# Optimization experiments

Hardware: AMD Instinct MI355X
Metric: run time of the kernel (lower is better)

Reference implementation:

```python
import jax, jax.numpy as jnp
import numpy as np

B, N, D, H, COND = 1, 1024, 1024, 16, 128
S = 2 * N          # noisy tokens + clean x0 tokens
BS = 16            # diffusion block size
HD = D // H        # head dim = 64


def _ln(x, w):
    # LayerNorm module: F.layer_norm in fp32, then scale by weight (no bias)
    x = x.astype(jnp.float32)
    mu = jnp.mean(x, axis=-1, keepdims=True)
    var = jnp.var(x, axis=-1, keepdims=True)
    return (x - mu) / jnp.sqrt(var + 1e-5) * w


def _rotate_half(x):
    x1, x2 = jnp.split(x, 2, axis=-1)
    return jnp.concatenate([-x2, x1], axis=-1)


def _block_diff_mask(s, n, bs):
    q = jnp.arange(s)[:, None]
    k = jnp.arange(s)[None, :]
    fq = q >= n
    fk = k >= n
    bq = jnp.where(fq, (q - n) // bs, q // bs)
    bk = jnp.where(fk, (k - n) // bs, k // bs)
    diag = (bq == bk) & (fq == fk)
    off = (bq > bk) & fk & (~fq)
    caus = (bq >= bk) & fk & fq
    return diag | off | caus


def setup_inputs() -> dict:
    key = jax.random.key(0)
    ks = jax.random.split(key, 8)
    inv = 1.0 / (10000.0 ** (jnp.arange(0, HD, 2, dtype=jnp.float32) / HD))  # [32]
    t = jnp.arange(N, dtype=jnp.float32)[:, None] * inv[None, :]
    return {
        "x": jax.random.normal(ks[0], (B, S, D), jnp.float32),
        "c": jax.random.normal(ks[1], (B, COND), jnp.float32),
        "cos": jnp.cos(t),
        "sin": jnp.sin(t),
        "norm1_w": jnp.ones((D,), jnp.float32),
        "qkv_w": jax.random.normal(ks[2], (3 * D, D), jnp.float32) * (D ** -0.5),
        "attn_out_w": jax.random.normal(ks[3], (D, D), jnp.float32) * (D ** -0.5),
        "norm2_w": jnp.ones((D,), jnp.float32),
        "mlp_w1": jax.random.normal(ks[4], (4 * D, D), jnp.float32) * (D ** -0.5),
        "mlp_b1": jnp.zeros((4 * D,), jnp.float32),
        "mlp_w2": jax.random.normal(ks[5], (D, 4 * D), jnp.float32) * ((4 * D) ** -0.5),
        "mlp_b2": jnp.zeros((D,), jnp.float32),
        "adaLN_w": jax.random.normal(ks[6], (6 * D, COND), jnp.float32) * 0.02,
        "adaLN_b": jax.random.normal(ks[7], (6 * D,), jnp.float32) * 0.02,
    }


def reference(x, c, cos, sin, norm1_w, qkv_w, attn_out_w, norm2_w,
              mlp_w1, mlp_b1, mlp_w2, mlp_b2, adaLN_w, adaLN_b):
    # adaLN modulation: [B, 6D] -> six [B, 1, D] tensors
    mods = (c @ adaLN_w.T + adaLN_b)[:, None, :]
    sh_msa, sc_msa, g_msa, sh_mlp, sc_mlp, g_mlp = jnp.split(mods, 6, axis=-1)

    x_skip = x
    h = _ln(x, norm1_w) * (1 + sc_msa) + sh_msa  # modulate_fused

    # rotary tables broadcast to qkv rank 5 (torchscript path: applied to q, k AND v)
    cs = jnp.concatenate([cos, cos], axis=-1)[None, :, None, None, :]  # [1,N,1,1,HD]
    sn = jnp.concatenate([sin, sin], axis=-1)[None, :, None, None, :]

    def qkv_of(xh):  # xh: [B, N, D]
        qkv = (xh @ qkv_w.T).reshape(B, N, 3, H, HD)
        return qkv * cs + _rotate_half(qkv) * sn

    # halves processed separately (both use positions 0..N-1), then concatenated
    qkv = jnp.concatenate([qkv_of(h[:, :N]), qkv_of(h[:, N:])], axis=1)  # [B,S,3,H,HD]

    q = jnp.transpose(qkv[:, :, 0], (0, 2, 1, 3))  # [B,H,S,HD]
    k = jnp.transpose(qkv[:, :, 1], (0, 2, 1, 3))
    v = jnp.transpose(qkv[:, :, 2], (0, 2, 1, 3))

    scores = jnp.einsum('bhqd,bhkd->bhqk', q, k) / np.sqrt(HD).astype(np.float32)
    mask = _block_diff_mask(S, N, BS)  # [S,S] bool, block-diag | offset-causal | block-causal
    scores = jnp.where(mask[None, None], scores, -jnp.inf)
    attn = jax.nn.softmax(scores, axis=-1)
    o = jnp.einsum('bhqk,bhkd->bhqd', attn, v)
    o = jnp.transpose(o, (0, 2, 1, 3)).reshape(B, S, D)

    # inference bias_dropout_add_scale: gate * out + residual (dropout is identity)
    x2 = g_msa * (o @ attn_out_w.T) + x_skip
    h2 = _ln(x2, norm2_w) * (1 + sc_mlp) + sh_mlp
    m = jax.nn.gelu(h2 @ mlp_w1.T + mlp_b1, approximate=True) @ mlp_w2.T + mlp_b2
    return g_mlp * m + x2
```

## Files before the change

### kernel.cpp

```cpp
#include <hip/hip_runtime.h>
#include <math.h>

#define SS 2048
#define NN 1024
#define DD 1024
#define HH 16
#define CONDD 128

typedef unsigned short ushort;
typedef unsigned int uint;
typedef __bf16 bf16x8 __attribute__((ext_vector_type(8)));
typedef float f32x4 __attribute__((ext_vector_type(4)));
typedef short s16x4 __attribute__((ext_vector_type(4)));
typedef ushort u16x8 __attribute__((ext_vector_type(8)));

__device__ __forceinline__ float gelu_fast(float x) {
    float t = x + 0.044715f * x * x * x;
    float e = __builtin_exp2f(-2.3022081446f * t);
    return x * __builtin_amdgcn_rcpf(1.0f + e);
}

__device__ __forceinline__ ushort f2bf(float x) {
    uint u = __float_as_uint(x);
    u += 0x7fff + ((u >> 16) & 1);
    return (ushort)(u >> 16);
}

__device__ __forceinline__ float bf2f(ushort u) {
    return __uint_as_float(((uint)u) << 16);
}

__device__ __forceinline__ void gload16(const ushort* g, ushort* l) {
    __builtin_amdgcn_global_load_lds(
        (const __attribute__((address_space(1))) void*)g,
        (__attribute__((address_space(3))) void*)l, 16, 0, 0);
}

template <int N>
__device__ __forceinline__ void wait_vm() {
    if constexpr (N == 0)      asm volatile("s_waitcnt vmcnt(0)" ::: "memory");
    else if constexpr (N == 4) asm volatile("s_waitcnt vmcnt(4)" ::: "memory");
    else if constexpr (N == 6) asm volatile("s_waitcnt vmcnt(6)" ::: "memory");
    else if constexpr (N == 8) asm volatile("s_waitcnt vmcnt(8)" ::: "memory");
}

__device__ __forceinline__ f32x4 mfma16(s16x4 a, s16x4 b, f32x4 c) {
#if __has_builtin(__builtin_amdgcn_mfma_f32_16x16x16bf16_1k)
    return __builtin_amdgcn_mfma_f32_16x16x16bf16_1k(a, b, c, 0, 0, 0);
#else
    asm("v_mfma_f32_16x16x16_bf16 %0, %1, %2, %0" : "+v"(c) : "v"(a), "v"(b));
    return c;
#endif
}

__global__ void k_cast4(const float* __restrict__ s0, const float* __restrict__ s1,
                        const float* __restrict__ s2, const float* __restrict__ s3,
                        ushort* __restrict__ dst) {
    size_t gid = ((size_t)blockIdx.x * 256 + threadIdx.x) * 4;
    const float* src;
    size_t off;
    if (gid < (3ull << 20))      { src = s0; off = 0; }
    else if (gid < (4ull << 20)) { src = s1; off = 3ull << 20; }
    else if (gid < (8ull << 20)) { src = s2; off = 4ull << 20; }
    else                         { src = s3; off = 8ull << 20; }
    float4 v = *(const float4*)(src + (gid - off));
    ushort4 o = {f2bf(v.x), f2bf(v.y), f2bf(v.z), f2bf(v.w)};
    *(ushort4*)(dst + gid) = o;
}

__global__ void k_adaln(const float* __restrict__ c, const float* __restrict__ w,
                        const float* __restrict__ b, float* __restrict__ mods) {
    int o = blockIdx.x * 256 + threadIdx.x;
    float s = b[o];
    const float* wr = w + (size_t)o * CONDD;
    for (int k = 0; k < CONDD; ++k) s += c[k] * wr[k];
    mods[o] = s;
}

__global__ void k_ln_mod(const float* __restrict__ x, const float* __restrict__ w,
                         const float* __restrict__ mods, int sh_idx, int sc_idx,
                         ushort* __restrict__ out) {
    int row = blockIdx.x;
    int tid = threadIdx.x;
    const float* xr = x + (size_t)row * DD;
    float lx[4];
    float s = 0.f, s2 = 0.f;
    for (int i = 0; i < 4; ++i) {
        float v = xr[tid + i * 256];
        lx[i] = v; s += v; s2 += v * v;
    }
    __shared__ float rs[256], rs2[256];
    rs[tid] = s; rs2[tid] = s2; __syncthreads();
    for (int off = 128; off > 0; off >>= 1) {
        if (tid < off) { rs[tid] += rs[tid + off]; rs2[tid] += rs2[tid + off]; }
        __syncthreads();
    }
    float mu = rs[0] * (1.0f / DD);
    float var = rs2[0] * (1.0f / DD) - mu * mu;
    float rstd = rsqrtf(var + 1e-5f);
    const float* sh = mods + sh_idx * DD;
    const float* sc = mods + sc_idx * DD;
    ushort* orow = out + (size_t)row * DD;
    for (int i = 0; i < 4; ++i) {
        int d = tid + i * 256;
        orow[d] = f2bf((lx[i] - mu) * rstd * w[d] * (1.0f + sc[d]) + sh[d]);
    }
}

template <int TM, int TN, int MODE, typename OT>
__global__ void k_gemm_mfma(const ushort* __restrict__ A, const ushort* __restrict__ W,
                            const float* __restrict__ bias, const float* __restrict__ gate,
                            const float* __restrict__ resid, OT* __restrict__ C,
                            int M, int Nout, int K) {
    constexpr int WRows = (TN == 64) ? 2 : ((TM == 128) ? 2 : 1);
    constexpr int WCols = 4 / WRows;
    constexpr int WTM = TM / WRows, WTN = TN / WCols;
    constexpr int FM = WTM / 16, FN = WTN / 16;
    constexpr int BUFE = (TM + TN) * 64;
    constexpr int LPW = TM / 32 + TN / 32;
    __shared__ ushort lds[3 * BUFE];

    int tid = threadIdx.x;
    int lane = tid & 63, wave = tid >> 6;
    int wr = wave / WCols, wc = wave % WCols;
    int l15 = lane & 15, l4 = lane >> 4;

    int nwg = gridDim.x * gridDim.y;
    int orig = blockIdx.y * gridDim.x + blockIdx.x;
    int q = nwg >> 3, r = nwg & 7;
    int xcd = orig & 7, off = orig >> 3;
    int wgid = (xcd < r ? xcd * (q + 1) : r * (q + 1) + (xcd - r) * q) + off;
    int n0 = (wgid % gridDim.x) * TN;
    int m0 = (wgid / gridDim.x) * TM;

    f32x4 acc[FM][FN] = {};

    auto stage = [&](int buf, int k0) {
        ushort* base = lds + buf * BUFE;
#pragma unroll
        for (int i = 0; i < TM / 32; ++i) {
            int cb = (wave * (TM / 32) + i) * 64;
            int ch = cb + lane;
            int row = ch >> 3;
            int kc = (ch & 7) ^ (row & 7);
            gload16(A + (size_t)(m0 + row) * K + k0 + kc * 8, base + cb * 8);
        }
#pragma unroll
        for (int i = 0; i < TN / 32; ++i) {
            int cb = (wave * (TN / 32) + i) * 64;
            int ch = cb + lane;
            int row = ch >> 3;
            int kc = (ch & 7) ^ (row & 7);
            gload16(W + (size_t)(n0 + row) * K + k0 + kc * 8, base + TM * 64 + cb * 8);
        }
    };

    auto compute = [&](int buf) {
        const ushort* lA = lds + buf * BUFE;
        const ushort* lB = lA + TM * 64;
#pragma unroll
        for (int sub = 0; sub < 2; ++sub) {
            bf16x8 af[FM], bw[FN];
#pragma unroll
            for (int mi = 0; mi < FM; ++mi) {
                int row = wr * WTM + mi * 16 + l15;
                int pos = ((sub << 2) | l4) ^ (row & 7);
                af[mi] = *(const bf16x8*)&lA[row * 64 + pos * 8];
            }
#pragma unroll
            for (int ni = 0; ni < FN; ++ni) {
                int row = wc * WTN + ni * 16 + l15;
                int pos = ((sub << 2) | l4) ^ (row & 7);
                bw[ni] = *(const bf16x8*)&lB[row * 64 + pos * 8];
            }
#pragma unroll
            for (int mi = 0; mi < FM; ++mi)
#pragma unroll
                for (int ni = 0; ni < FN; ++ni)
                    acc[mi][ni] = __builtin_amdgcn_mfma_f32_16x16x32_bf16(
                        af[mi], bw[ni], acc[mi][ni], 0, 0, 0);
        }
    };

    int nk = K >> 6;
    stage(0, 0);
    stage(1, 64);
    for (int t = 0; t < nk; ++t) {
        if (t + 1 < nk) wait_vm<LPW>(); else wait_vm<0>();
        __builtin_amdgcn_s_barrier();
        __builtin_amdgcn_sched_barrier(0);
        if (t + 2 < nk) stage((t + 2) % 3, (t + 2) << 6);
        compute(t % 3);
    }

#pragma unroll
    for (int mi = 0; mi < FM; ++mi) {
#pragma unroll
        for (int r2 = 0; r2 < 4; ++r2) {
            int m = m0 + wr * WTM + mi * 16 + l4 * 4 + r2;
#pragma unroll
            for (int ni = 0; ni < FN; ++ni) {
                int n = n0 + wc * WTN + ni * 16 + l15;
                float v = acc[mi][ni][r2];
                if (MODE == 1) v = gate[n] * v + resid[(size_t)m * Nout + n];
                if (MODE == 2) v = gelu_fast(v + bias[n]);
                if (MODE == 3) v = gate[n] * (v + bias[n]) + resid[(size_t)m * Nout + n];
                if (sizeof(OT) == 2) C[(size_t)m * Nout + n] = (OT)f2bf(v);
                else                 C[(size_t)m * Nout + n] = (OT)v;
            }
        }
    }
}

__global__ void k_rope2(const ushort* __restrict__ qkvb, const float* __restrict__ cosT,
                        const float* __restrict__ sinT, ushort* __restrict__ qb,
                        ushort* __restrict__ kb, ushort* __restrict__ vT) {
    __shared__ ushort vt[64][65];
    int h = blockIdx.x & 15;
    int st = blockIdx.x >> 4;
    int s0 = st * 64;
    int tid = threadIdx.x;
#pragma unroll
    for (int i = 0; i < 8; ++i) {
        int idx = tid + i * 256;
        int sl = idx >> 5, j = idx & 31;
        int s = s0 + sl;
        int pos = s & (NN - 1);
        float cv = cosT[pos * 32 + j], sv = sinT[pos * 32 + j];
        const ushort* row = qkvb + (size_t)s * 3072 + h * 64;
        float x1 = bf2f(row[j]), x2 = bf2f(row[j + 32]);
        qb[(size_t)s * DD + h * 64 + j]      = f2bf((x1 * cv - x2 * sv) * 0.18033688011f);
        qb[(size_t)s * DD + h * 64 + j + 32] = f2bf((x2 * cv + x1 * sv) * 0.18033688011f);
        x1 = bf2f(row[1024 + j]); x2 = bf2f(row[1024 + j + 32]);
        kb[(size_t)s * DD + h * 64 + j]      = f2bf(x1 * cv - x2 * sv);
        kb[(size_t)s * DD + h * 64 + j + 32] = f2bf(x2 * cv + x1 * sv);
        x1 = bf2f(row[2048 + j]); x2 = bf2f(row[2048 + j + 32]);
        vt[sl][j]      = f2bf(x1 * cv - x2 * sv);
        vt[sl][j + 32] = f2bf(x2 * cv + x1 * sv);
    }
    __syncthreads();
    int drow = tid >> 2, sc = (tid & 3) * 16;
    u16x8 a, b;
#pragma unroll
    for (int i = 0; i < 8; ++i) { a[i] = vt[sc + i][drow]; b[i] = vt[sc + 8 + i][drow]; }
    size_t base = (size_t)(h * 64 + drow) * SS + s0 + sc;
    *(u16x8*)&vT[base] = a;
    *(u16x8*)&vT[base + 8] = b;
}

struct KVTile { bf16x8 k0, k1; s16x4 v0, v1, v2, v3; };

__global__ __launch_bounds__(256) void k_attn4(
        const ushort* __restrict__ qb, const ushort* __restrict__ kb,
        const ushort* __restrict__ vT, ushort* __restrict__ o) {
    __shared__ float Ml[2][4][16], Ll[2][4][16];
    __shared__ float Ob[2][4][16][68];

    int id = blockIdx.x;
    int h = id & 15;
    int bq = 63 - (id >> 4);
    int tid = threadIdx.x;
    int wave = tid >> 6;
    int lane = tid & 63;
    int l15 = lane & 15, l4 = lane >> 4;
    int hb = h * 64;

    const int q0A = bq * 16, q0B = NN + bq * 16;
    bf16x8 qA0 = *(const bf16x8*)&qb[(size_t)(q0A + l15) * DD + hb + l4 * 8];
    bf16x8 qA1 = *(const bf16x8*)&qb[(size_t)(q0A + l15) * DD + hb + 32 + l4 * 8];
    bf16x8 qB0 = *(const bf16x8*)&qb[(size_t)(q0B + l15) * DD + hb + l4 * 8];
    bf16x8 qB1 = *(const bf16x8*)&qb[(size_t)(q0B + l15) * DD + hb + 32 + l4 * 8];

    float mA = -1e30f, lA = 0.f, mB = -1e30f, lB = 0.f;
    f32x4 oA0 = {}, oA1 = {}, oA2 = {}, oA3 = {};
    f32x4 oB0 = {}, oB1 = {}, oB2 = {}, oB3 = {};

    auto loadT = [&](int kbase) {
        KVTile t;
        const ushort* kr = kb + (size_t)(kbase + l15) * DD + hb + l4 * 8;
        t.k0 = *(const bf16x8*)kr;
        t.k1 = *(const bf16x8*)(kr + 32);
        const ushort* vr = vT + (size_t)(hb + l15) * SS + kbase + l4 * 4;
        t.v0 = *(const s16x4*)vr;
        t.v1 = *(const s16x4*)(vr + 16 * SS);
        t.v2 = *(const s16x4*)(vr + 32 * SS);
        t.v3 = *(const s16x4*)(vr + 48 * SS);
        return t;
    };

    auto step = [&](const KVTile& t, bf16x8 Q0, bf16x8 Q1, float& m, float& l,
                    f32x4& O0, f32x4& O1, f32x4& O2, f32x4& O3) {
        f32x4 s = {};
        s = __builtin_amdgcn_mfma_f32_16x16x32_bf16(t.k0, Q0, s, 0, 0, 0);
        s = __builtin_amdgcn_mfma_f32_16x16x32_bf16(t.k1, Q1, s, 0, 0, 0);
        float tm = fmaxf(fmaxf(s[0], s[1]), fmaxf(s[2], s[3]));
        tm = fmaxf(tm, __shfl_xor(tm, 16));
        tm = fmaxf(tm, __shfl_xor(tm, 32));
        if (!__all(tm <= m + 8.0f)) {
            float mn = fmaxf(m, tm);
            float alpha = exp2f(m - mn);
            l *= alpha;
            O0 *= alpha; O1 *= alpha; O2 *= alpha; O3 *= alpha;
            m = mn;
        }
        float p0 = exp2f(s[0] - m), p1 = exp2f(s[1] - m);
        float p2 = exp2f(s[2] - m), p3 = exp2f(s[3] - m);
        float rsum = (p0 + p1) + (p2 + p3);
        rsum += __shfl_xor(rsum, 16);
        rsum += __shfl_xor(rsum, 32);
        l += rsum;
        s16x4 pf;
        pf[0] = (short)f2bf(p0); pf[1] = (short)f2bf(p1);
        pf[2] = (short)f2bf(p2); pf[3] = (short)f2bf(p3);
        O0 = mfma16(t.v0, pf, O0);
        O1 = mfma16(t.v1, pf, O1);
        O2 = mfma16(t.v2, pf, O2);
        O3 = mfma16(t.v3, pf, O3);
    };

    if (wave == 0) {
        KVTile td = loadT(q0A);
        step(td, qA0, qA1, mA, lA, oA0, oA1, oA2, oA3);
    }
    KVTile cur, nxt;
    if (wave <= bq) cur = loadT(NN + wave * 16);
    for (int t = wave; t <= bq; t += 4) {
        int tn = t + 4;
        if (tn <= bq) nxt = loadT(NN + tn * 16);
        if (t < bq) step(cur, qA0, qA1, mA, lA, oA0, oA1, oA2, oA3);
        step(cur, qB0, qB1, mB, lB, oB0, oB1, oB2, oB3);
        cur = nxt;
    }

    if (l4 == 0) {
        Ml[0][wave][l15] = mA; Ll[0][wave][l15] = lA;
        Ml[1][wave][l15] = mB; Ll[1][wave][l15] = lB;
    }
    *(f32x4*)&Ob[0][wave][l15][l4 * 4]      = oA0;
    *(f32x4*)&Ob[0][wave][l15][l4 * 4 + 16] = oA1;
    *(f32x4*)&Ob[0][wave][l15][l4 * 4 + 32] = oA2;
    *(f32x4*)&Ob[0][wave][l15][l4 * 4 + 48] = oA3;
    *(f32x4*)&Ob[1][wave][l15][l4 * 4]      = oB0;
    *(f32x4*)&Ob[1][wave][l15][l4 * 4 + 16] = oB1;
    *(f32x4*)&Ob[1][wave][l15][l4 * 4 + 32] = oB2;
    *(f32x4*)&Ob[1][wave][l15][l4 * 4 + 48] = oB3;
    __syncthreads();

    int s = tid >> 7;
    int qr = (tid >> 3) & 15;
    int db = (tid & 7) * 8;
    float m0 = Ml[s][0][qr], m1 = Ml[s][1][qr], m2 = Ml[s][2][qr], m3 = Ml[s][3][qr];
    float ms = fmaxf(fmaxf(m0, m1), fmaxf(m2, m3));
    float a0 = exp2f(m0 - ms), a1 = exp2f(m1 - ms);
    float a2 = exp2f(m2 - ms), a3 = exp2f(m3 - ms);
    float lt = a0 * Ll[s][0][qr] + a1 * Ll[s][1][qr] + a2 * Ll[s][2][qr] + a3 * Ll[s][3][qr];
    float inv = 1.0f / lt;
    int q0s = (s == 0) ? q0A : q0B;
    u16x8 outv;
#pragma unroll
    for (int j = 0; j < 8; ++j) {
        float v = a0 * Ob[s][0][qr][db + j] + a1 * Ob[s][1][qr][db + j] +
                  a2 * Ob[s][2][qr][db + j] + a3 * Ob[s][3][qr][db + j];
        outv[j] = f2bf(v * inv);
    }
    *(u16x8*)&o[(size_t)(q0s + qr) * DD + hb + db] = outv;
}

extern "C" void kernel_launch(void* const* d_in, const int* in_sizes, int n_in,
                              void* d_out, int out_size, void* d_ws, size_t ws_size,
                              hipStream_t stream) {
    const float* x          = (const float*)d_in[0];
    const float* c          = (const float*)d_in[1];
    const float* cosT       = (const float*)d_in[2];
    const float* sinT       = (const float*)d_in[3];
    const float* norm1_w    = (const float*)d_in[4];
    const float* qkv_w      = (const float*)d_in[5];
    const float* attn_out_w = (const float*)d_in[6];
    const float* norm2_w    = (const float*)d_in[7];
    const float* mlp_w1     = (const float*)d_in[8];
    const float* mlp_b1     = (const float*)d_in[9];
    const float* mlp_w2     = (const float*)d_in[10];
    const float* mlp_b2     = (const float*)d_in[11];
    const float* adaLN_w    = (const float*)d_in[12];
    const float* adaLN_b    = (const float*)d_in[13];
    float* out = (float*)d_out;

    char* p = (char*)d_ws;
    float*  mods = (float*)p;   p += 6 * DD * 4;
    ushort* qkvb = (ushort*)p;  p += (size_t)SS * 3 * DD * 2;
    ushort* qb   = (ushort*)p;  p += (size_t)SS * DD * 2;
    ushort* kb   = (ushort*)p;  p += (size_t)SS * DD * 2;
    ushort* vT   = (ushort*)p;  p += (size_t)SS * DD * 2;
    float*  x2   = (float*)p;   p += (size_t)SS * DD * 4;
    ushort* hbuf = (ushort*)p;  p += (size_t)SS * DD * 2;
    ushort* obuf = (ushort*)p;  p += (size_t)SS * DD * 2;
    ushort* wq   = (ushort*)p;  p += (size_t)3 * DD * DD * 2;
    ushort* wo   = (ushort*)p;  p += (size_t)DD * DD * 2;
    ushort* w1   = (ushort*)p;  p += (size_t)4 * DD * DD * 2;
    ushort* w2   = (ushort*)p;  p += (size_t)4 * DD * DD * 2;
    ushort* m1   = qkvb;

    k_cast4<<<(12 << 20) / 1024, 256, 0, stream>>>(qkv_w, attn_out_w, mlp_w1, mlp_w2, wq);

    k_adaln<<<6 * DD / 256, 256, 0, stream>>>(c, adaLN_w, adaLN_b, mods);
    k_ln_mod<<<SS, 256, 0, stream>>>(x, norm1_w, mods, 0, 1, hbuf);

    dim3 g1(3 * DD / 128, SS / 64);
    k_gemm_mfma<64, 128, 0, ushort><<<g1, 256, 0, stream>>>(
        hbuf, wq, nullptr, nullptr, nullptr, qkvb, SS, 3 * DD, DD);
    k_rope2<<<512, 256, 0, stream>>>(qkvb, cosT, sinT, qb, kb, vT);
    k_attn4<<<HH * 64, 256, 0, stream>>>(qb, kb, vT, obuf);

    dim3 g2(DD / 64, SS / 64);
    k_gemm_mfma<64, 64, 1, float><<<g2, 256, 0, stream>>>(
        obuf, wo, nullptr, mods + 2 * DD, x, x2, SS, DD, DD);
    k_ln_mod<<<SS, 256, 0, stream>>>(x2, norm2_w, mods, 3, 4, hbuf);

    dim3 g3(4 * DD / 128, SS / 64);
    k_gemm_mfma<64, 128, 2, ushort><<<g3, 256, 0, stream>>>(
        hbuf, w1, mlp_b1, nullptr, nullptr, m1, SS, 4 * DD, DD);
    dim3 g4(DD / 64, SS / 64);
    k_gemm_mfma<64, 64, 3, float><<<g4, 256, 0, stream>>>(
        m1, w2, mlp_b2, mods + 5 * DD, x2, out, SS, DD, 4 * DD);
}
```

Measured before the change: 162.2 us.

## Use 8-wave GEMM workgroups and store attention residual as bf16

The GEMM kernel now runs 512 threads (2x4 waves) per workgroup, so each wave owns a smaller output sub-tile and issues fewer staging loads per K-step. The wait counts are adjusted to match. The intermediate residual x2 is written as bf16 instead of fp32, which halves its write traffic and the reads by the second LayerNorm and the final GEMM. In exchange the residual stream loses precision, and smaller per-wave tiles reduce MFMA reuse per LDS fragment load.

```diff
diff --git a/kernel.cpp b/kernel.cpp
--- a/kernel.cpp
+++ b/kernel.cpp
@@ -30,6 +30,9 @@
     return __uint_as_float(((uint)u) << 16);
 }
 
+__device__ __forceinline__ float ldf(const float* p) { return *p; }
+__device__ __forceinline__ float ldf(const ushort* p) { return bf2f(*p); }
+
 __device__ __forceinline__ void gload16(const ushort* g, ushort* l) {
     __builtin_amdgcn_global_load_lds(
         (const __attribute__((address_space(1))) void*)g,
@@ -39,9 +42,8 @@
 template <int N>
 __device__ __forceinline__ void wait_vm() {
     if constexpr (N == 0)      asm volatile("s_waitcnt vmcnt(0)" ::: "memory");
-    else if constexpr (N == 4) asm volatile("s_waitcnt vmcnt(4)" ::: "memory");
-    else if constexpr (N == 6) asm volatile("s_waitcnt vmcnt(6)" ::: "memory");
-    else if constexpr (N == 8) asm volatile("s_waitcnt vmcnt(8)" ::: "memory");
+    else if constexpr (N == 2) asm volatile("s_waitcnt vmcnt(2)" ::: "memory");
+    else if constexpr (N == 3) asm volatile("s_waitcnt vmcnt(3)" ::: "memory");
 }
 
 __device__ __forceinline__ f32x4 mfma16(s16x4 a, s16x4 b, f32x4 c) {
@@ -77,16 +79,17 @@
     mods[o] = s;
 }
 
-__global__ void k_ln_mod(const float* __restrict__ x, const float* __restrict__ w,
+template <typename IT>
+__global__ void k_ln_mod(const IT* __restrict__ x, const float* __restrict__ w,
                          const float* __restrict__ mods, int sh_idx, int sc_idx,
                          ushort* __restrict__ out) {
     int row = blockIdx.x;
     int tid = threadIdx.x;
-    const float* xr = x + (size_t)row * DD;
+    const IT* xr = x + (size_t)row * DD;
     float lx[4];
     float s = 0.f, s2 = 0.f;
     for (int i = 0; i < 4; ++i) {
-        float v = xr[tid + i * 256];
+        float v = ldf(&xr[tid + i * 256]);
         lx[i] = v; s += v; s2 += v * v;
     }
     __shared__ float rs[256], rs2[256];
@@ -108,21 +111,20 @@
 }
 
 template <int TM, int TN, int MODE, typename OT>
-__global__ void k_gemm_mfma(const ushort* __restrict__ A, const ushort* __restrict__ W,
-                            const float* __restrict__ bias, const float* __restrict__ gate,
-                            const float* __restrict__ resid, OT* __restrict__ C,
-                            int M, int Nout, int K) {
-    constexpr int WRows = (TN == 64) ? 2 : ((TM == 128) ? 2 : 1);
-    constexpr int WCols = 4 / WRows;
-    constexpr int WTM = TM / WRows, WTN = TN / WCols;
+__global__ __launch_bounds__(512) void k_gemm_mfma(
+        const ushort* __restrict__ A, const ushort* __restrict__ W,
+        const float* __restrict__ bias, const float* __restrict__ gate,
+        const void* __restrict__ resid, OT* __restrict__ C,
+        int M, int Nout, int K) {
+    constexpr int WTM = TM / 2, WTN = TN / 4;
     constexpr int FM = WTM / 16, FN = WTN / 16;
     constexpr int BUFE = (TM + TN) * 64;
-    constexpr int LPW = TM / 32 + TN / 32;
+    constexpr int LPW = TM / 64 + TN / 64;
     __shared__ ushort lds[3 * BUFE];
 
     int tid = threadIdx.x;
     int lane = tid & 63, wave = tid >> 6;
-    int wr = wave / WCols, wc = wave % WCols;
+    int wr = wave >> 2, wc = wave & 3;
     int l15 = lane & 15, l4 = lane >> 4;
 
     int nwg = gridDim.x * gridDim.y;
@@ -138,16 +140,16 @@
     auto stage = [&](int buf, int k0) {
         ushort* base = lds + buf * BUFE;
 #pragma unroll
-        for (int i = 0; i < TM / 32; ++i) {
-            int cb = (wave * (TM / 32) + i) * 64;
+        for (int i = 0; i < TM / 64; ++i) {
+            int cb = (wave * (TM / 64) + i) * 64;
             int ch = cb + lane;
             int row = ch >> 3;
             int kc = (ch & 7) ^ (row & 7);
             gload16(A + (size_t)(m0 + row) * K + k0 + kc * 8, base + cb * 8);
         }
 #pragma unroll
-        for (int i = 0; i < TN / 32; ++i) {
-            int cb = (wave * (TN / 32) + i) * 64;
+        for (int i = 0; i < TN / 64; ++i) {
+            int cb = (wave * (TN / 64) + i) * 64;
             int ch = cb + lane;
             int row = ch >> 3;
             int kc = (ch & 7) ^ (row & 7);
@@ -193,6 +195,8 @@
         compute(t % 3);
     }
 
+    const float*  rf = (const float*)resid;
+    const ushort* rb = (const ushort*)resid;
 #pragma unroll
     for (int mi = 0; mi < FM; ++mi) {
 #pragma unroll
@@ -202,9 +206,9 @@
             for (int ni = 0; ni < FN; ++ni) {
                 int n = n0 + wc * WTN + ni * 16 + l15;
                 float v = acc[mi][ni][r2];
-                if (MODE == 1) v = gate[n] * v + resid[(size_t)m * Nout + n];
+                if (MODE == 1) v = gate[n] * v + rf[(size_t)m * Nout + n];
                 if (MODE == 2) v = gelu_fast(v + bias[n]);
-                if (MODE == 3) v = gate[n] * (v + bias[n]) + resid[(size_t)m * Nout + n];
+                if (MODE == 3) v = gate[n] * (v + bias[n]) + bf2f(rb[(size_t)m * Nout + n]);
                 if (sizeof(OT) == 2) C[(size_t)m * Nout + n] = (OT)f2bf(v);
                 else                 C[(size_t)m * Nout + n] = (OT)v;
             }
@@ -391,7 +395,7 @@
     ushort* qb   = (ushort*)p;  p += (size_t)SS * DD * 2;
     ushort* kb   = (ushort*)p;  p += (size_t)SS * DD * 2;
     ushort* vT   = (ushort*)p;  p += (size_t)SS * DD * 2;
-    float*  x2   = (float*)p;   p += (size_t)SS * DD * 4;
+    ushort* x2b  = (ushort*)p;  p += (size_t)SS * DD * 2;
     ushort* hbuf = (ushort*)p;  p += (size_t)SS * DD * 2;
     ushort* obuf = (ushort*)p;  p += (size_t)SS * DD * 2;
     ushort* wq   = (ushort*)p;  p += (size_t)3 * DD * DD * 2;
@@ -403,23 +407,23 @@
     k_cast4<<<(12 << 20) / 1024, 256, 0, stream>>>(qkv_w, attn_out_w, mlp_w1, mlp_w2, wq);
 
     k_adaln<<<6 * DD / 256, 256, 0, stream>>>(c, adaLN_w, adaLN_b, mods);
-    k_ln_mod<<<SS, 256, 0, stream>>>(x, norm1_w, mods, 0, 1, hbuf);
+    k_ln_mod<float><<<SS, 256, 0, stream>>>(x, norm1_w, mods, 0, 1, hbuf);
 
     dim3 g1(3 * DD / 128, SS / 64);
-    k_gemm_mfma<64, 128, 0, ushort><<<g1, 256, 0, stream>>>(
+    k_gemm_mfma<64, 128, 0, ushort><<<g1, 512, 0, stream>>>(
         hbuf, wq, nullptr, nullptr, nullptr, qkvb, SS, 3 * DD, DD);
     k_rope2<<<512, 256, 0, stream>>>(qkvb, cosT, sinT, qb, kb, vT);
     k_attn4<<<HH * 64, 256, 0, stream>>>(qb, kb, vT, obuf);
 
     dim3 g2(DD / 64, SS / 64);
-    k_gemm_mfma<64, 64, 1, float><<<g2, 256, 0, stream>>>(
-        obuf, wo, nullptr, mods + 2 * DD, x, x2, SS, DD, DD);
-    k_ln_mod<<<SS, 256, 0, stream>>>(x2, norm2_w, mods, 3, 4, hbuf);
+    k_gemm_mfma<64, 64, 1, ushort><<<g2, 512, 0, stream>>>(
+        obuf, wo, nullptr, mods + 2 * DD, x, x2b, SS, DD, DD);
+    k_ln_mod<ushort><<<SS, 256, 0, stream>>>(x2b, norm2_w, mods, 3, 4, hbuf);
 
     dim3 g3(4 * DD / 128, SS / 64);
-    k_gemm_mfma<64, 128, 2, ushort><<<g3, 256, 0, stream>>>(
+    k_gemm_mfma<64, 128, 2, ushort><<<g3, 512, 0, stream>>>(
         hbuf, w1, mlp_b1, nullptr, nullptr, m1, SS, 4 * DD, DD);
     dim3 g4(DD / 64, SS / 64);
-    k_gemm_mfma<64, 64, 3, float><<<g4, 256, 0, stream>>>(
-        m1, w2, mlp_b2, mods + 5 * DD, x2, out, SS, DD, 4 * DD);
-}
+    k_gemm_mfma<64, 64, 3, float><<<g4, 512, 0, stream>>>(
+        m1, w2, mlp_b2, mods + 5 * DD, x2b, out, SS, DD, 4 * DD);
+}
```

Result: no change. 163.6 us (+0.9%).
